# Performance work log

Hardware: AMD Instinct MI355X
Metric: run time of the kernel (lower is better)

## Reference

```python
import jax, jax.numpy as jnp
import numpy as np

B, MBS, F, CD = 512, 32768, 512, 16  # batch, mini_batch_size, filter_length, cond_dim

def setup_inputs() -> dict:
    key = jax.random.key(0)
    ks = jax.random.split(key, 8)
    return {
        "inputs": jax.random.normal(ks[0], (B, MBS, 1), jnp.float32),
        "c": jax.random.normal(ks[1], (B, 1, CD), jnp.float32),
        "W0": jax.random.normal(ks[2], (CD, F), jnp.float32) * 0.1,
        "b0": jnp.zeros((F,), jnp.float32),
        "alpha": jnp.full((F,), 0.25, jnp.float32),
        "Wg": jax.random.normal(ks[3], (CD, F), jnp.float32) * 0.1,
        "bg": jnp.zeros((F,), jnp.float32),
        "Wb": jax.random.normal(ks[4], (CD, F), jnp.float32) * 0.1,
        "bb": jnp.zeros((F,), jnp.float32),
        "Wglu": jax.random.normal(ks[5], (F, 2 * F), jnp.float32) * 0.05,
        "bglu": jnp.zeros((2 * F,), jnp.float32),
        "Wf": jax.random.normal(ks[6], (F, F), jnp.float32) * 0.05,
        "bf": jnp.zeros((F,), jnp.float32),
    }

def reference(inputs, c, W0, b0, alpha, Wg, bg, Wb, bb, Wglu, bglu, Wf, bf):
    mbs = inputs.shape[1]
    flen = Wf.shape[1]
    # conditioning stack: Dense -> PReLU -> FiLM -> GLU -> Dense(softsign)
    c_ = c @ W0 + b0                                  # [B,1,F]
    c_ = jnp.where(c_ >= 0, c_, alpha * c_)           # PReLU
    c_ = c_ * (c @ Wg + bg) + (c @ Wb + bb)           # FiLM
    g = c_ @ Wglu + bglu                              # [B,1,2F]
    a, gate = jnp.split(g, 2, axis=-1)
    c_ = a * jax.nn.sigmoid(gate)                     # GLU
    filters = jax.nn.soft_sign(c_ @ Wf + bf)          # [B,1,F]
    # FFT-based circular (linear via zero pad) convolution
    conv_len = mbs + flen - 1
    X = jnp.fft.fft(inputs[:, :, 0].astype(jnp.complex64), n=conv_len)   # [B,conv_len]
    H = jnp.fft.fft(filters[:, 0, :].astype(jnp.complex64), n=conv_len)  # [B,conv_len]
    y = jnp.fft.ifft(X * H)
    return jnp.real(y[:, :mbs])                       # [B,MBS]
```

## Files before the change

kernel.cpp:

```cpp
#include <hip/hip_runtime.h>


typedef float f32x16 __attribute__((ext_vector_type(16)));
typedef float f32x4  __attribute__((ext_vector_type(4)));
typedef __bf16 bf16x8 __attribute__((ext_vector_type(8)));

__device__ __forceinline__ unsigned short f2bf(float f) {
    unsigned int u = __float_as_uint(f);
    u += 0x7FFFu + ((u >> 16) & 1u);
    return (unsigned short)(u >> 16);
}

__device__ __forceinline__ uint4 pack8n(float4 a, float4 b) {
    bf16x8 v;
    v[0] = (__bf16)a.x; v[1] = (__bf16)a.y; v[2] = (__bf16)a.z; v[3] = (__bf16)a.w;
    v[4] = (__bf16)b.x; v[5] = (__bf16)b.y; v[6] = (__bf16)b.z; v[7] = (__bf16)b.w;
    uint4 r;
    __builtin_memcpy(&r, &v, 16);
    return r;
}

__global__ __launch_bounds__(256) void kA(
    const float* __restrict__ Wglu, const float* __restrict__ Wf,
    const float* __restrict__ c, const float* __restrict__ W0,
    const float* __restrict__ b0, const float* __restrict__ alpha,
    const float* __restrict__ Wg, const float* __restrict__ bg,
    const float* __restrict__ Wb, const float* __restrict__ bb,
    unsigned short* __restrict__ WgluT, unsigned short* __restrict__ WfT,
    unsigned short* __restrict__ cfilm) {
    const int blk = blockIdx.x, tid = threadIdx.x;
    if (blk < 192) {
        __shared__ float ldsF[64 * 65];
        const float* src; unsigned short* dst; int tj, tk, srcld;
        if (blk < 128) { tj = blk >> 3; tk = blk & 7; src = Wglu; dst = WgluT; srcld = 1024; }
        else { int b2 = blk - 128; tj = b2 >> 3; tk = b2 & 7; src = Wf; dst = WfT; srcld = 512; }
#pragma unroll
        for (int rr = 0; rr < 16; ++rr) {
            int kl = (tid >> 6) + (rr << 2), jl = tid & 63;
            ldsF[kl * 65 + jl] = src[(size_t)(tk * 64 + kl) * srcld + tj * 64 + jl];
        }
        __syncthreads();
#pragma unroll
        for (int rr = 0; rr < 16; ++rr) {
            int jl = (tid >> 6) + (rr << 2), kl = tid & 63;
            dst[(size_t)(tj * 64 + jl) * 512 + tk * 64 + kl] = f2bf(ldsF[kl * 65 + jl]);
        }
    } else {
        int id = (blk - 192) * 256 + tid;
        int b = id >> 9, f = id & 511;
        const float* cb = c + b * 16;
        float d0 = 0.f, dg = 0.f, db = 0.f;
#pragma unroll
        for (int i = 0; i < 16; ++i) {
            float cv = cb[i];
            d0 += cv * W0[i * 512 + f];
            dg += cv * Wg[i * 512 + f];
            db += cv * Wb[i * 512 + f];
        }
        float pre = d0 + b0[f];
        float pr = pre >= 0.f ? pre : alpha[f] * pre;
        float v = pr * (dg + bg[f]) + (db + bb[f]);
        cfilm[id] = f2bf(v);
    }
}

__global__ __launch_bounds__(256) void k2_glu(
    const unsigned short* __restrict__ cfilm, const unsigned short* __restrict__ WgluT,
    const float* __restrict__ bglu, unsigned short* __restrict__ cglu) {
    int wid = (blockIdx.x * 256 + threadIdx.x) >> 6;
    int l = threadIdx.x & 63;
    int tm = wid >> 5, tn = wid & 31;
    int row = tm * 16 + (l & 15);
    int col = tn * 16 + (l & 15);
    int kh = 8 * (l >> 4);
    f32x4 accA, accG;
#pragma unroll
    for (int i = 0; i < 4; ++i) { accA[i] = 0.f; accG[i] = 0.f; }
    const unsigned short* ap  = cfilm + row * 512 + kh;
    const unsigned short* bap = WgluT + col * 512 + kh;
    const unsigned short* bgp = WgluT + (512 + col) * 512 + kh;
#pragma unroll
    for (int kc = 0; kc < 16; ++kc) {
        bf16x8 a   = *(const bf16x8*)(ap  + kc * 32);
        bf16x8 ba  = *(const bf16x8*)(bap + kc * 32);
        bf16x8 bgt = *(const bf16x8*)(bgp + kc * 32);
        accA = __builtin_amdgcn_mfma_f32_16x16x32_bf16(a, ba,  accA, 0, 0, 0);
        accG = __builtin_amdgcn_mfma_f32_16x16x32_bf16(a, bgt, accG, 0, 0, 0);
    }
    float biasA = bglu[col], biasG = bglu[512 + col];
#pragma unroll
    for (int r = 0; r < 4; ++r) {
        float ga = accA[r] + biasA;
        float gg = accG[r] + biasG;
        float s = 1.f / (1.f + expf(-gg));
        int m = (l >> 4) * 4 + r;
        cglu[(tm * 16 + m) * 512 + col] = f2bf(ga * s);
    }
}

__global__ __launch_bounds__(256) void k3_filt(
    const unsigned short* __restrict__ cglu, const unsigned short* __restrict__ WfT,
    const float* __restrict__ bfv, unsigned short* __restrict__ hout) {
    int wid = (blockIdx.x * 256 + threadIdx.x) >> 6;
    int l = threadIdx.x & 63;
    int tm = wid >> 5, tn = wid & 31;
    int row = tm * 16 + (l & 15);
    int col = tn * 16 + (l & 15);
    int kh = 8 * (l >> 4);
    f32x4 acc;
#pragma unroll
    for (int i = 0; i < 4; ++i) acc[i] = 0.f;
    const unsigned short* ap = cglu + row * 512 + kh;
    const unsigned short* bp = WfT + col * 512 + kh;
#pragma unroll
    for (int kc = 0; kc < 16; ++kc) {
        bf16x8 a  = *(const bf16x8*)(ap + kc * 32);
        bf16x8 bv = *(const bf16x8*)(bp + kc * 32);
        acc = __builtin_amdgcn_mfma_f32_16x16x32_bf16(a, bv, acc, 0, 0, 0);
    }
    float bias = bfv[col];
#pragma unroll
    for (int r = 0; r < 4; ++r) {
        float z = acc[r] + bias;
        float h = z / (1.f + fabsf(z));
        int m = (l >> 4) * 4 + r;
        hout[(tm * 16 + m) * 512 + col] = f2bf(h);
    }
}

__global__ __launch_bounds__(256, 2) void k5(
    const float* __restrict__ x, const unsigned short* __restrict__ hbf,
    float* __restrict__ y) {
    __shared__ __align__(16) unsigned char smem[45184];
    const int tid = threadIdx.x;
    const int b = blockIdx.x;
    const float* xb = x + (size_t)b * 32768;
    unsigned short* hs = (unsigned short*)(smem + 44160);

    ((unsigned int*)hs)[tid] = ((const unsigned int*)(hbf + (size_t)b * 512))[tid];
    __syncthreads();

    for (int e = tid; e < 8 * 292; e += 256) {
        int s = e / 292, w = e - s * 292;
        int j0 = 2 * w + s;
        unsigned int v0 = (j0 >= 32 && j0 < 544) ? hs[543 - j0] : 0u;
        unsigned int v1 = (j0 >= 31 && j0 < 543) ? hs[542 - j0] : 0u;
        ((unsigned int*)(smem + 34816))[e] = v0 | (v1 << 16);
    }

#pragma unroll
    for (int r = 0; r < 5; ++r) {
        int slot = tid + (r << 8);
        if (slot < 1088) {
            int g = slot - 64;
            uint4 w4;
            if (g >= 0) {
                float4 a  = *(const float4*)(xb + g * 8);
                float4 b2 = *(const float4*)(xb + g * 8 + 4);
                w4 = pack8n(a, b2);
            } else {
                w4 = make_uint4(0u, 0u, 0u, 0u);
            }
            *(uint4*)(smem + ((slot ^ ((slot >> 3) & 7)) << 4)) = w4;
        }
    }
    __syncthreads();

    const int w = tid >> 6, l = tid & 63;
    const int q = l & 31, hl = l >> 5;
    const int lq = 4 * q + hl;
    const int abase = 66 + (w << 8) + lq;
    const int o0 = 559 - q + 8 * hl;
    const int s8 = o0 & 7;
    const unsigned char* hrb = smem + 34816 + s8 * 1168 + ((o0 - s8) << 1);

    for (int c = 0; c < 4; ++c) {
        const unsigned char* wb = smem + ((c & 1) ? 17408 : 0);
        unsigned char* sb = smem + ((c & 1) ? 0 : 17408);
        float4 La0, La1, La2, La3, La4, Lb0, Lb1, Lb2, Lb3, Lb4;
        if (c < 3) {
            const float* px = xb + (((c + 1) << 13) - 512);
            La0 = *(const float4*)(px + (tid << 3));           Lb0 = *(const float4*)(px + (tid << 3) + 4);
            La1 = *(const float4*)(px + ((tid + 256) << 3));   Lb1 = *(const float4*)(px + ((tid + 256) << 3) + 4);
            La2 = *(const float4*)(px + ((tid + 512) << 3));   Lb2 = *(const float4*)(px + ((tid + 512) << 3) + 4);
            La3 = *(const float4*)(px + ((tid + 768) << 3));   Lb3 = *(const float4*)(px + ((tid + 768) << 3) + 4);
            if (tid < 64) {
                La4 = *(const float4*)(px + ((tid + 1024) << 3));
                Lb4 = *(const float4*)(px + ((tid + 1024) << 3) + 4);
            }
        }
        f32x16 acc0, acc1;
#pragma unroll
        for (int i = 0; i < 16; ++i) { acc0[i] = 0.f; acc1[i] = 0.f; }
#pragma unroll
        for (int cc = 0; cc < 17; ++cc) {
            bf16x8 bfr = *(const bf16x8*)(hrb - (cc << 5));
            int a0 = abase - 2 * cc, a1 = a0 + 128;
            bf16x8 xa0 = *(const bf16x8*)(wb + ((a0 ^ ((a0 >> 3) & 7)) << 4));
            bf16x8 xa1 = *(const bf16x8*)(wb + ((a1 ^ ((a1 >> 3) & 7)) << 4));
            acc0 = __builtin_amdgcn_mfma_f32_32x32x16_bf16(xa0, bfr, acc0, 0, 0, 0);
            acc1 = __builtin_amdgcn_mfma_f32_32x32x16_bf16(xa1, bfr, acc1, 0, 0, 0);
        }
        if (c < 3) {
            int s0 = tid;
            *(uint4*)(sb + ((s0 ^ ((s0 >> 3) & 7)) << 4)) = pack8n(La0, Lb0);
            int s1 = tid + 256;
            *(uint4*)(sb + ((s1 ^ ((s1 >> 3) & 7)) << 4)) = pack8n(La1, Lb1);
            int s2 = tid + 512;
            *(uint4*)(sb + ((s2 ^ ((s2 >> 3) & 7)) << 4)) = pack8n(La2, Lb2);
            int s3 = tid + 768;
            *(uint4*)(sb + ((s3 ^ ((s3 >> 3) & 7)) << 4)) = pack8n(La3, Lb3);
            if (tid < 64) {
                int s4 = tid + 1024;
                *(uint4*)(sb + ((s4 ^ ((s4 >> 3) & 7)) << 4)) = pack8n(La4, Lb4);
            }
        }
#pragma unroll
        for (int cc = 17; cc < 34; ++cc) {
            bf16x8 bfr = *(const bf16x8*)(hrb - (cc << 5));
            int a0 = abase - 2 * cc, a1 = a0 + 128;
            bf16x8 xa0 = *(const bf16x8*)(wb + ((a0 ^ ((a0 >> 3) & 7)) << 4));
            bf16x8 xa1 = *(const bf16x8*)(wb + ((a1 ^ ((a1 >> 3) & 7)) << 4));
            acc0 = __builtin_amdgcn_mfma_f32_32x32x16_bf16(xa0, bfr, acc0, 0, 0, 0);
            acc1 = __builtin_amdgcn_mfma_f32_32x32x16_bf16(xa1, bfr, acc1, 0, 0, 0);
        }
        asm volatile("s_waitcnt lgkmcnt(0)" ::: "memory");
        __builtin_amdgcn_s_barrier();
        __builtin_amdgcn_sched_barrier(0);
        float* yb = y + (size_t)b * 32768 + (c << 13) + (w << 11) + q;
#pragma unroll
        for (int r = 0; r < 16; ++r) {
            int m = (r & 3) + 8 * (r >> 2) + 4 * hl;
            yb[m << 5] = acc0[r];
            yb[1024 + (m << 5)] = acc1[r];
        }
    }
}

extern "C" void kernel_launch(void* const* d_in, const int* in_sizes, int n_in,
                              void* d_out, int out_size, void* d_ws, size_t ws_size,
                              hipStream_t stream) {
    const float* x    = (const float*)d_in[0];
    const float* c    = (const float*)d_in[1];
    const float* W0   = (const float*)d_in[2];
    const float* b0   = (const float*)d_in[3];
    const float* al   = (const float*)d_in[4];
    const float* Wg   = (const float*)d_in[5];
    const float* bg   = (const float*)d_in[6];
    const float* Wb   = (const float*)d_in[7];
    const float* bb   = (const float*)d_in[8];
    const float* Wglu = (const float*)d_in[9];
    const float* bglu = (const float*)d_in[10];
    const float* Wf   = (const float*)d_in[11];
    const float* bf   = (const float*)d_in[12];
    float* y = (float*)d_out;

    char* ws = (char*)d_ws;
    unsigned short* cfilm = (unsigned short*)(ws);
    unsigned short* WgluT = (unsigned short*)(ws + 524288);
    unsigned short* WfT   = (unsigned short*)(ws + 1572864);
    unsigned short* cglu  = (unsigned short*)(ws + 2097152);
    unsigned short* hbf   = (unsigned short*)(ws + 2621440);

    kA<<<dim3(1216), dim3(256), 0, stream>>>(Wglu, Wf, c, W0, b0, al, Wg, bg, Wb, bb,
                                             WgluT, WfT, cfilm);
    k2_glu<<<dim3(256), dim3(256), 0, stream>>>(cfilm, WgluT, bglu, cglu);
    k3_filt<<<dim3(256), dim3(256), 0, stream>>>(cglu, WfT, bf, hbf);
    k5<<<dim3(512), dim3(256), 0, stream>>>(x, hbf, y);
}
```

Measured before the change: 49.55 us.

## Split each batch row's convolution across two blocks with smaller tiles

The conv kernel now launches two blocks per batch row, each covering half of the 32768 outputs in four chunks of 4096. Each wave computes one 32x32 MFMA accumulator instead of two, shared memory drops to about 28.8KB, and launch bounds allow four blocks per CU. The goal is more blocks and better occupancy on a 256-CU part, where 512 blocks left it underfilled. In exchange, the filter Toeplitz setup and the 512-sample halo load are repeated per block, and each wave has less MFMA work per LDS read.

```diff
diff --git a/kernel.cpp b/kernel.cpp
--- a/kernel.cpp
+++ b/kernel.cpp
@@ -128,14 +128,15 @@
     }
 }
 
-__global__ __launch_bounds__(256, 2) void k5(
+__global__ __launch_bounds__(256, 4) void k6(
     const float* __restrict__ x, const unsigned short* __restrict__ hbf,
     float* __restrict__ y) {
-    __shared__ __align__(16) unsigned char smem[45184];
+    __shared__ __align__(16) unsigned char smem[28800];
     const int tid = threadIdx.x;
-    const int b = blockIdx.x;
+    const int b = blockIdx.x >> 1;
+    const int n0 = (blockIdx.x & 1) << 14;
     const float* xb = x + (size_t)b * 32768;
-    unsigned short* hs = (unsigned short*)(smem + 44160);
+    unsigned short* hs = (unsigned short*)(smem + 27776);
 
     ((unsigned int*)hs)[tid] = ((const unsigned int*)(hbf + (size_t)b * 512))[tid];
     __syncthreads();
@@ -145,18 +146,18 @@
         int j0 = 2 * w + s;
         unsigned int v0 = (j0 >= 32 && j0 < 544) ? hs[543 - j0] : 0u;
         unsigned int v1 = (j0 >= 31 && j0 < 543) ? hs[542 - j0] : 0u;
-        ((unsigned int*)(smem + 34816))[e] = v0 | (v1 << 16);
-    }
-
-#pragma unroll
-    for (int r = 0; r < 5; ++r) {
-        int slot = tid + (r << 8);
-        if (slot < 1088) {
-            int g = slot - 64;
+        ((unsigned int*)(smem + 18432))[e] = v0 | (v1 << 16);
+    }
+
+#pragma unroll
+    for (int r2 = 0; r2 < 3; ++r2) {
+        int slot = tid + (r2 << 8);
+        if (slot < 576) {
+            int off = n0 + ((slot - 64) << 3);
             uint4 w4;
-            if (g >= 0) {
-                float4 a  = *(const float4*)(xb + g * 8);
-                float4 b2 = *(const float4*)(xb + g * 8 + 4);
+            if (off >= 0) {
+                float4 a  = *(const float4*)(xb + off);
+                float4 b2 = *(const float4*)(xb + off + 4);
                 w4 = pack8n(a, b2);
             } else {
                 w4 = make_uint4(0u, 0u, 0u, 0u);
@@ -169,70 +170,59 @@
     const int w = tid >> 6, l = tid & 63;
     const int q = l & 31, hl = l >> 5;
     const int lq = 4 * q + hl;
-    const int abase = 66 + (w << 8) + lq;
+    const int abase = 66 + (w << 7) + lq;
     const int o0 = 559 - q + 8 * hl;
     const int s8 = o0 & 7;
-    const unsigned char* hrb = smem + 34816 + s8 * 1168 + ((o0 - s8) << 1);
+    const unsigned char* hrb = smem + 18432 + s8 * 1168 + ((o0 - s8) << 1);
 
     for (int c = 0; c < 4; ++c) {
-        const unsigned char* wb = smem + ((c & 1) ? 17408 : 0);
-        unsigned char* sb = smem + ((c & 1) ? 0 : 17408);
-        float4 La0, La1, La2, La3, La4, Lb0, Lb1, Lb2, Lb3, Lb4;
+        const unsigned char* wb = smem + ((c & 1) ? 9216 : 0);
+        unsigned char* sb = smem + ((c & 1) ? 0 : 9216);
+        float4 La0, Lb0, La1, Lb1, La2, Lb2;
         if (c < 3) {
-            const float* px = xb + (((c + 1) << 13) - 512);
-            La0 = *(const float4*)(px + (tid << 3));           Lb0 = *(const float4*)(px + (tid << 3) + 4);
-            La1 = *(const float4*)(px + ((tid + 256) << 3));   Lb1 = *(const float4*)(px + ((tid + 256) << 3) + 4);
-            La2 = *(const float4*)(px + ((tid + 512) << 3));   Lb2 = *(const float4*)(px + ((tid + 512) << 3) + 4);
-            La3 = *(const float4*)(px + ((tid + 768) << 3));   Lb3 = *(const float4*)(px + ((tid + 768) << 3) + 4);
+            const float* px = xb + n0 + ((c + 1) << 12) - 512;
+            La0 = *(const float4*)(px + (tid << 3));         Lb0 = *(const float4*)(px + (tid << 3) + 4);
+            La1 = *(const float4*)(px + ((tid + 256) << 3)); Lb1 = *(const float4*)(px + ((tid + 256) << 3) + 4);
             if (tid < 64) {
-                La4 = *(const float4*)(px + ((tid + 1024) << 3));
-                Lb4 = *(const float4*)(px + ((tid + 1024) << 3) + 4);
+                La2 = *(const float4*)(px + ((tid + 512) << 3));
+                Lb2 = *(const float4*)(px + ((tid + 512) << 3) + 4);
             }
         }
-        f32x16 acc0, acc1;
-#pragma unroll
-        for (int i = 0; i < 16; ++i) { acc0[i] = 0.f; acc1[i] = 0.f; }
+        f32x16 acc;
+#pragma unroll
+        for (int i = 0; i < 16; ++i) acc[i] = 0.f;
 #pragma unroll
         for (int cc = 0; cc < 17; ++cc) {
             bf16x8 bfr = *(const bf16x8*)(hrb - (cc << 5));
-            int a0 = abase - 2 * cc, a1 = a0 + 128;
-            bf16x8 xa0 = *(const bf16x8*)(wb + ((a0 ^ ((a0 >> 3) & 7)) << 4));
-            bf16x8 xa1 = *(const bf16x8*)(wb + ((a1 ^ ((a1 >> 3) & 7)) << 4));
-            acc0 = __builtin_amdgcn_mfma_f32_32x32x16_bf16(xa0, bfr, acc0, 0, 0, 0);
-            acc1 = __builtin_amdgcn_mfma_f32_32x32x16_bf16(xa1, bfr, acc1, 0, 0, 0);
+            int a0 = abase - 2 * cc;
+            bf16x8 xa = *(const bf16x8*)(wb + ((a0 ^ ((a0 >> 3) & 7)) << 4));
+            acc = __builtin_amdgcn_mfma_f32_32x32x16_bf16(xa, bfr, acc, 0, 0, 0);
         }
         if (c < 3) {
             int s0 = tid;
             *(uint4*)(sb + ((s0 ^ ((s0 >> 3) & 7)) << 4)) = pack8n(La0, Lb0);
             int s1 = tid + 256;
             *(uint4*)(sb + ((s1 ^ ((s1 >> 3) & 7)) << 4)) = pack8n(La1, Lb1);
-            int s2 = tid + 512;
-            *(uint4*)(sb + ((s2 ^ ((s2 >> 3) & 7)) << 4)) = pack8n(La2, Lb2);
-            int s3 = tid + 768;
-            *(uint4*)(sb + ((s3 ^ ((s3 >> 3) & 7)) << 4)) = pack8n(La3, Lb3);
             if (tid < 64) {
-                int s4 = tid + 1024;
-                *(uint4*)(sb + ((s4 ^ ((s4 >> 3) & 7)) << 4)) = pack8n(La4, Lb4);
+                int s2 = tid + 512;
+                *(uint4*)(sb + ((s2 ^ ((s2 >> 3) & 7)) << 4)) = pack8n(La2, Lb2);
             }
         }
 #pragma unroll
         for (int cc = 17; cc < 34; ++cc) {
             bf16x8 bfr = *(const bf16x8*)(hrb - (cc << 5));
-            int a0 = abase - 2 * cc, a1 = a0 + 128;
-            bf16x8 xa0 = *(const bf16x8*)(wb + ((a0 ^ ((a0 >> 3) & 7)) << 4));
-            bf16x8 xa1 = *(const bf16x8*)(wb + ((a1 ^ ((a1 >> 3) & 7)) << 4));
-            acc0 = __builtin_amdgcn_mfma_f32_32x32x16_bf16(xa0, bfr, acc0, 0, 0, 0);
-            acc1 = __builtin_amdgcn_mfma_f32_32x32x16_bf16(xa1, bfr, acc1, 0, 0, 0);
+            int a0 = abase - 2 * cc;
+            bf16x8 xa = *(const bf16x8*)(wb + ((a0 ^ ((a0 >> 3) & 7)) << 4));
+            acc = __builtin_amdgcn_mfma_f32_32x32x16_bf16(xa, bfr, acc, 0, 0, 0);
         }
         asm volatile("s_waitcnt lgkmcnt(0)" ::: "memory");
         __builtin_amdgcn_s_barrier();
         __builtin_amdgcn_sched_barrier(0);
-        float* yb = y + (size_t)b * 32768 + (c << 13) + (w << 11) + q;
+        float* yb = y + (size_t)b * 32768 + n0 + (c << 12) + (w << 10) + q;
 #pragma unroll
         for (int r = 0; r < 16; ++r) {
             int m = (r & 3) + 8 * (r >> 2) + 4 * hl;
-            yb[m << 5] = acc0[r];
-            yb[1024 + (m << 5)] = acc1[r];
+            yb[m << 5] = acc[r];
         }
     }
 }
@@ -266,5 +256,5 @@
                                              WgluT, WfT, cfilm);
     k2_glu<<<dim3(256), dim3(256), 0, stream>>>(cfilm, WgluT, bglu, cglu);
     k3_filt<<<dim3(256), dim3(256), 0, stream>>>(cglu, WfT, bf, hbf);
-    k5<<<dim3(512), dim3(256), 0, stream>>>(x, hbf, y);
-}
+    k6<<<dim3(1024), dim3(256), 0, stream>>>(x, hbf, y);
+}
```

Measured after the change: 52.01 us. 5.0% more time.
